# Performance work log

Hardware: AMD Instinct MI355X
Metric: run time of the kernel (lower is better)

## Reference

```python
import jax, jax.numpy as jnp
import numpy as np

EPS = 1e-5
GROUPS = 4


def gconv1x1(x, w, b, groups):
    # x: [B,C,H,W]; w: [Cout, Cin//groups]; grouped 1x1 conv
    B, C, H, W = x.shape
    Co = w.shape[0]
    xg = x.reshape(B, groups, C // groups, H, W)
    wg = w.reshape(groups, Co // groups, C // groups)
    y = jnp.einsum('bgchw,goc->bgohw', xg, wg).reshape(B, Co, H, W)
    if b is not None:
        y = y + b[None, :, None, None]
    return y


def setup_inputs() -> dict:
    key = jax.random.key(0)
    ks = jax.random.split(key, 9)
    B, C, H, W = 8, 64, 160, 160
    Cq = C // 8
    s = 0.1
    return {
        'x': jax.random.normal(ks[0], (B, C, H, W), jnp.float32),
        'wq': jax.random.normal(ks[1], (Cq, C // GROUPS), jnp.float32) * s,
        'bq': jax.random.normal(ks[2], (Cq,), jnp.float32) * s,
        'wk': jax.random.normal(ks[3], (Cq, C // GROUPS), jnp.float32) * s,
        'bk': jax.random.normal(ks[4], (Cq,), jnp.float32) * s,
        'wv': jax.random.normal(ks[5], (C, C // GROUPS), jnp.float32) * s,
        'bv': jax.random.normal(ks[6], (C,), jnp.float32) * s,
        'gamma': jax.random.normal(ks[7], (1,), jnp.float32) * s,
        'w1d': jax.random.normal(ks[8], (C, C // GROUPS), jnp.float32) * s,
        'bn_w': jnp.ones((C,), jnp.float32),
        'bn_b': jnp.zeros((C,), jnp.float32),
    }


def reference(x, wq, bq, wk, bk, wv, bv, gamma, w1d, bn_w, bn_b):
    B, C, H, W = x.shape
    q = gconv1x1(x, wq, bq, GROUPS)   # [B,Cq,H,W]
    k = gconv1x1(x, wk, bk, GROUPS)   # [B,Cq,H,W]
    v = gconv1x1(x, wv, bv, GROUPS)   # [B,C,H,W]

    # column (H) attention energies with -inf diagonal (self excluded on H path)
    energy_H = jnp.einsum('bchw,bcjw->bhwj', q, k)  # [B,H,W,H]
    diag = jnp.where(jnp.eye(H, dtype=bool), -jnp.inf, 0.0).astype(x.dtype)
    energy_H = energy_H + diag[:, None, :]
    # row (W) attention energies
    energy_W = jnp.einsum('bchw,bchj->bhwj', q, k)  # [B,H,W,W]

    att = jax.nn.softmax(jnp.concatenate([energy_H, energy_W], axis=3), axis=3)
    att_H = att[..., :H]           # [B,H,W,H]
    att_W = att[..., H:]           # [B,H,W,W]

    out_H = jnp.einsum('bcjw,bhwj->bchw', v, att_H)
    out_W = jnp.einsum('bchj,bhwj->bchw', v, att_W)
    out = gamma[0] * (out_H + out_W)               # [B,C,H,W]

    # kernel-size-1 grouped conv1d (dilation irrelevant for k=1), no bias
    L = H * W
    o = out.reshape(B, GROUPS, C // GROUPS, L)
    w1g = w1d.reshape(GROUPS, C // GROUPS, C // GROUPS)
    o = jnp.einsum('bgcl,goc->bgol', o, w1g).reshape(B, C, L)

    # BatchNorm1d (training mode: batch stats over (B, L), biased variance)
    mean = jnp.mean(o, axis=(0, 2), keepdims=True)
    var = jnp.mean((o - mean) ** 2, axis=(0, 2), keepdims=True)
    o = (o - mean) / jnp.sqrt(var + EPS) * bn_w[None, :, None] + bn_b[None, :, None]

    o = o.reshape(B, C, H, W)
    return jax.nn.relu(o + x)
```

## Files before the change

kernel.cpp:

```cpp
#include <hip/hip_runtime.h>
#include <math.h>

#define B_ 8
#define C_ 64
#define H_ 160
#define W_ 160
#define HW_ (H_*W_)

typedef _Float16 h2 __attribute__((ext_vector_type(2)));
typedef _Float16 h4 __attribute__((ext_vector_type(4)));
typedef _Float16 h8 __attribute__((ext_vector_type(8)));
typedef float f4v __attribute__((ext_vector_type(4)));
union H8u { h8 v; h2 h[4]; };

__device__ inline float fdot2(h2 a, h2 b, float c) {
    return __builtin_amdgcn_fdot2(a, b, c, false);
}

#define LOG2E 1.44269504088896f
#define ESH2  5.77078016355585f
#if __has_builtin(__builtin_amdgcn_exp2f)
#define EXP2F(x) __builtin_amdgcn_exp2f(x)
#else
#define EXP2F(x) exp2f(x)
#endif

__device__ inline void cvtw16(const float* wp, float sc, H8u& a, H8u& b) {
    #pragma unroll
    for (int j = 0; j < 4; j++) {
        float4 f = ((const float4*)wp)[j];
        h2 lo, hi;
        lo.x = (_Float16)(f.x*sc); lo.y = (_Float16)(f.y*sc);
        hi.x = (_Float16)(f.z*sc); hi.y = (_Float16)(f.w*sc);
        if (j < 2) { a.h[(j&1)*2] = lo; a.h[(j&1)*2+1] = hi; }
        else       { b.h[(j&1)*2] = lo; b.h[(j&1)*2+1] = hi; }
    }
}

static constexpr size_t N_PIX  = (size_t)B_*H_*W_;
static constexpr size_t N_FULL = (size_t)B_*H_*W_*C_;
static constexpr size_t OFF_OUTH  = 0;
static constexpr size_t OFF_VROW  = N_FULL/2;
static constexpr size_t OFF_QROW  = OFF_VROW + N_FULL/2;
static constexpr size_t OFF_KROW  = OFF_QROW + N_PIX*4;
static constexpr size_t OFF_MH    = OFF_KROW + N_PIX*4;
static constexpr size_t OFF_SH    = OFF_MH + N_PIX;
static constexpr size_t OFF_BNSUM = OFF_SH + N_PIX;
static constexpr size_t OFF_BNSQ  = OFF_BNSUM + 64;

__global__ __launch_bounds__(256,4) void qkv_kernel(
    const float* __restrict__ x,
    const float* __restrict__ wq, const float* __restrict__ bq,
    const float* __restrict__ wk, const float* __restrict__ bk,
    const float* __restrict__ wv, const float* __restrict__ bv,
    _Float16* __restrict__ qrow, _Float16* __restrict__ krow,
    _Float16* __restrict__ vrow)
{
    __shared__ __align__(16) _Float16 spool[10240];
    _Float16 (*xsh)[72] = (_Float16 (*)[72])spool;

    const int tid = threadIdx.x;
    const int w0 = blockIdx.x * 32;
    const int h0 = blockIdx.y * 4;
    const int b  = blockIdx.z;

    const float* xb = x + (size_t)b*C_*HW_;
    for (int i = tid; i < 2048; i += 256) {
        int w4 = i & 7;
        int c  = ((i >> 3) & 7) | (((i >> 6) & 7) << 3);
        int hh = i >> 9;
        float4 v = *(const float4*)(xb + (size_t)c*HW_ + (size_t)(h0+hh)*W_ + w0 + w4*4);
        int pix = hh*32 + w4*4;
        xsh[pix+0][c] = (_Float16)v.x; xsh[pix+1][c] = (_Float16)v.y;
        xsh[pix+2][c] = (_Float16)v.z; xsh[pix+3][c] = (_Float16)v.w;
    }
    __syncthreads();

    float resv[32];
    {
        const int cp = tid & 31, pg = tid >> 5;
        const int c0 = 2*cp, g = c0 >> 4;
        H8u wa0, wb0, wa1, wb1;
        cvtw16(wv + c0*16,     1.0f, wa0, wb0);
        cvtw16(wv + (c0+1)*16, 1.0f, wa1, wb1);
        const float b0 = bv[c0], b1 = bv[c0+1];
        #pragma unroll 4
        for (int i = 0; i < 16; i++) {
            int pix = pg*16 + i;
            H8u x0; x0.v = *(const h8*)&xsh[pix][g*16];
            H8u x1; x1.v = *(const h8*)&xsh[pix][g*16 + 8];
            float s0 = b0, s1 = b1;
            #pragma unroll
            for (int j = 0; j < 4; j++) {
                s0 = fdot2(x0.h[j], wa0.h[j], s0);
                s1 = fdot2(x0.h[j], wa1.h[j], s1);
            }
            #pragma unroll
            for (int j = 0; j < 4; j++) {
                s0 = fdot2(x1.h[j], wb0.h[j], s0);
                s1 = fdot2(x1.h[j], wb1.h[j], s1);
            }
            resv[2*i] = s0; resv[2*i+1] = s1;
        }
    }
    float resqk[8];
    {
        const int out = tid & 15, pg = tid >> 4;
        const int cq = out & 7, g = cq >> 1;
        const float sc = (out < 8) ? LOG2E : 1.0f;
        const float* wp = ((out < 8) ? wq : wk) + cq*16;
        const float bb = ((out < 8) ? bq[cq] : bk[cq]) * sc;
        H8u qa, qb;
        cvtw16(wp, sc, qa, qb);
        #pragma unroll
        for (int i = 0; i < 8; i++) {
            int pix = pg*8 + i;
            H8u x0; x0.v = *(const h8*)&xsh[pix][g*16];
            H8u x1; x1.v = *(const h8*)&xsh[pix][g*16 + 8];
            float s = bb;
            #pragma unroll
            for (int j = 0; j < 4; j++) s = fdot2(x0.h[j], qa.h[j], s);
            #pragma unroll
            for (int j = 0; j < 4; j++) s = fdot2(x1.h[j], qb.h[j], s);
            resqk[i] = s;
        }
    }
    __syncthreads();

    unsigned* vs32 = (unsigned*)spool;
    unsigned* qk32 = vs32 + 4096;
    {
        const int cp = tid & 31, pg = tid >> 5;
        #pragma unroll
        for (int i = 0; i < 16; i++) {
            int pix = pg*16 + i;
            h2 p; p.x = (_Float16)resv[2*i]; p.y = (_Float16)resv[2*i+1];
            vs32[pix*32 + cp] = *(unsigned*)&p;
        }
    }
    {
        const int out = tid & 15, pg = tid >> 4;
        _Float16* qks = (_Float16*)qk32;
        #pragma unroll
        for (int i = 0; i < 8; i++) qks[(pg*8+i)*16 + out] = (_Float16)resqk[i];
    }
    __syncthreads();

    unsigned* vrow32 = (unsigned*)vrow;
    for (int i = tid; i < 4096; i += 256) {
        int pix = i >> 5, cp = i & 31;
        size_t bp = ((size_t)b*H_ + h0 + (pix>>5))*W_ + w0 + (pix & 31);
        vrow32[bp*32 + cp] = vs32[i];
    }
    unsigned* qrow32 = (unsigned*)qrow;
    unsigned* krow32 = (unsigned*)krow;
    for (int i = tid; i < 1024; i += 256) {
        int pix = i >> 3, part = i & 7;
        size_t bp = ((size_t)b*H_ + h0 + (pix>>5))*W_ + w0 + (pix & 31);
        unsigned val = qk32[pix*8 + part];
        if (part < 4) qrow32[bp*4 + part]     = val;
        else          krow32[bp*4 + part - 4] = val;
    }
}

__global__ __launch_bounds__(256,4) void passA_kernel(
    const _Float16* __restrict__ qrow, const _Float16* __restrict__ krow,
    const _Float16* __restrict__ vrow,
    _Float16* __restrict__ outH, float* __restrict__ sH)
{
    __shared__ __align__(16) _Float16 pool[10240];
    __shared__ __align__(16) _Float16 q2h[160][8];
    __shared__ __align__(16) _Float16 k2h[160][8];

    _Float16* v2s = pool;

    const int tid = threadIdx.x;
    const int b = blockIdx.x / W_;
    const int w = blockIdx.x % W_;

    if (tid < 160) {
        size_t bp = ((size_t)b*H_ + tid)*W_ + w;
        *(int4*)&q2h[tid][0] = *(const int4*)(qrow + bp*8);
        *(int4*)&k2h[tid][0] = *(const int4*)(krow + bp*8);
    }
    {
        const unsigned* vr32 = (const unsigned*)vrow;
        const int cp = tid & 31, hp0 = tid >> 5;
        #pragma unroll 5
        for (int it = 0; it < 10; it++) {
            int hp = hp0 + 8*it;
            int kt = hp >> 4, dqv = (hp >> 2) & 3, jj = 2*(hp & 3);
            size_t bp0 = ((size_t)b*H_ + 2*hp)*W_ + w;
            unsigned u0 = vr32[bp0*32 + cp];
            unsigned u1 = vr32[(bp0 + W_)*32 + cp];
            unsigned e  = __builtin_amdgcn_perm(u1, u0, 0x05040100);
            unsigned o  = __builtin_amdgcn_perm(u1, u0, 0x07060302);
            int base = ((kt*4 + dqv)*64 + 2*cp)*8 + jj;
            *(unsigned*)&v2s[base]     = e;
            *(unsigned*)&v2s[base + 8] = o;
        }
    }
    __syncthreads();

    const int u    = tid & 7;
    const int wl   = tid >> 3;
    const int lane = tid & 63;
    const int wid  = tid >> 6;
    const int cM   = wid*16 + (lane & 15);
    const int m_   = lane & 15;
    const int dq   = lane >> 4;

    h8 vfr[5];
    #pragma unroll
    for (int kt = 0; kt < 5; kt++)
        vfr[kt] = *(const h8*)&v2s[((kt*4 + dq)*64 + cM)*8];
    __syncthreads();

    for (int t = 0; t <= 5; t++) {
        if (t <= 4) {
            _Float16* Pts = pool + (t & 1)*5120;
            const int qh = t*32 + wl;
            H8u qr; qr.v = *(const h8*)&q2h[qh][0];
            float sloc = 0.f;
            #pragma unroll
            for (int p = 0; p < 10; p++) {
                int j0 = 2*u + 16*p;
                H8u ka; ka.v = *(const h8*)&k2h[j0][0];
                H8u kb; kb.v = *(const h8*)&k2h[j0+1][0];
                float e0 = 0.f, e1 = 0.f;
                #pragma unroll
                for (int i = 0; i < 4; i++) {
                    e0 = fdot2(qr.h[i], ka.h[i], e0);
                    e1 = fdot2(qr.h[i], kb.h[i], e1);
                }
                float p0 = (j0   == qh) ? 0.f : EXP2F(e0 - ESH2);
                float p1 = (j0+1 == qh) ? 0.f : EXP2F(e1 - ESH2);
                sloc += p0 + p1;
                h2 pp; pp.x = (_Float16)p0; pp.y = (_Float16)p1;
                int idx = (((p>>1)*4 + (u>>2) + 2*(p&1))*32 + wl)*8 + 2*(u&3);
                *(unsigned*)&Pts[idx] = *(unsigned*)&pp;
            }
            sloc += __shfl_xor(sloc, 1);
            sloc += __shfl_xor(sloc, 2);
            sloc += __shfl_xor(sloc, 4);
            if (u == 0) sH[((size_t)b*W_ + w)*H_ + qh] = sloc;
        }
        if (t >= 1) {
            const _Float16* Pts = pool + ((t-1) & 1)*5120;
            f4v acc0 = {0.f,0.f,0.f,0.f}, acc1 = {0.f,0.f,0.f,0.f};
            #pragma unroll
            for (int kt = 0; kt < 5; kt++) {
                h8 a0  = *(const h8*)&Pts[((kt*4 + dq)*32 + m_)*8];
                h8 a1  = *(const h8*)&Pts[((kt*4 + dq)*32 + 16 + m_)*8];
                acc0 = __builtin_amdgcn_mfma_f32_16x16x32_f16(a0, vfr[kt], acc0, 0, 0, 0);
                acc1 = __builtin_amdgcn_mfma_f32_16x16x32_f16(a1, vfr[kt], acc1, 0, 0, 0);
            }
            #pragma unroll
            for (int r = 0; r < 4; r++) {
                int r0 = (t-1)*32 + dq*4 + r;
                outH[(((size_t)b*H_ + r0     )*W_ + w)*64 + cM] = (_Float16)acc0[r];
                outH[(((size_t)b*H_ + r0 + 16)*W_ + w)*64 + cM] = (_Float16)acc1[r];
            }
        }
        if (t <= 4) __syncthreads();
    }
}

__global__ __launch_bounds__(256,4) void passB_kernel(
    const _Float16* __restrict__ qrow, const _Float16* __restrict__ krow,
    const _Float16* vrow,
    const float* __restrict__ gamma, const float* __restrict__ w1d,
    const _Float16* __restrict__ outH, const float* __restrict__ sH,
    _Float16* o16, float* __restrict__ bnsum, float* __restrict__ bnsq)
{
    __shared__ __align__(16) _Float16 pool[10240];
    __shared__ __align__(16) _Float16 stageh[4*32*20];
    __shared__ __align__(16) _Float16 q2h[160][8];
    __shared__ __align__(16) _Float16 k2h[160][8];
    __shared__ float fs[2][32];

    _Float16* v2s = pool;

    const int tid = threadIdx.x;
    const int b = blockIdx.x / H_;
    const int h = blockIdx.x % H_;
    const float gam = gamma[0];

    const int lane = tid & 63;
    const int wid  = tid >> 6;
    const int cM   = wid*16 + (lane & 15);
    const int m_   = lane & 15;
    const int dq   = lane >> 4;

    h4 w1f;
    {
        float4 wv4 = *(const float4*)(w1d + cM*16 + 4*dq);
        w1f[0] = (_Float16)wv4.x; w1f[1] = (_Float16)wv4.y;
        w1f[2] = (_Float16)wv4.z; w1f[3] = (_Float16)wv4.w;
    }

    const size_t rowbase = ((size_t)b*H_ + h)*W_;
    if (tid < 160) {
        size_t bp = rowbase + tid;
        *(int4*)&q2h[tid][0] = *(const int4*)(qrow + bp*8);
        *(int4*)&k2h[tid][0] = *(const int4*)(krow + bp*8);
    }
    {
        const unsigned* vr32 = (const unsigned*)vrow;
        const int cp = tid & 31, wp0 = tid >> 5;
        #pragma unroll 5
        for (int it = 0; it < 10; it++) {
            int wp = wp0 + 8*it;
            int kt = wp >> 4, dqv = (wp >> 2) & 3, jj = 2*(wp & 3);
            size_t bp0 = rowbase + 2*wp;
            unsigned u0 = vr32[bp0*32 + cp];
            unsigned u1 = vr32[(bp0 + 1)*32 + cp];
            unsigned e  = __builtin_amdgcn_perm(u1, u0, 0x05040100);
            unsigned o  = __builtin_amdgcn_perm(u1, u0, 0x07060302);
            int base = ((kt*4 + dqv)*64 + 2*cp)*8 + jj;
            *(unsigned*)&v2s[base]     = e;
            *(unsigned*)&v2s[base + 8] = o;
        }
    }
    __syncthreads();

    const int u  = tid & 7;
    const int wl = tid >> 3;

    h8 vfr[5];
    #pragma unroll
    for (int kt = 0; kt < 5; kt++)
        vfr[kt] = *(const h8*)&v2s[((kt*4 + dq)*64 + cM)*8];
    __syncthreads();

    float bnS = 0.f, bnS2 = 0.f;

    for (int t = 0; t <= 5; t++) {
        float oh0[4], oh1[4];
        if (t >= 1) {
            #pragma unroll
            for (int r = 0; r < 4; r++) {
                int rw0 = (t-1)*32 + dq*4 + r;
                oh0[r] = (float)outH[(rowbase + rw0     )*64 + cM];
                oh1[r] = (float)outH[(rowbase + rw0 + 16)*64 + cM];
            }
        }
        if (t <= 4) {
            _Float16* Pts = pool + (t & 1)*5120;
            const int qw = t*32 + wl;
            H8u qr; qr.v = *(const h8*)&q2h[qw][0];
            float sloc = 0.f;
            #pragma unroll
            for (int p = 0; p < 10; p++) {
                int j0 = 2*u + 16*p;
                H8u ka; ka.v = *(const h8*)&k2h[j0][0];
                H8u kb; kb.v = *(const h8*)&k2h[j0+1][0];
                float e0 = 0.f, e1 = 0.f;
                #pragma unroll
                for (int i = 0; i < 4; i++) {
                    e0 = fdot2(qr.h[i], ka.h[i], e0);
                    e1 = fdot2(qr.h[i], kb.h[i], e1);
                }
                float p0 = EXP2F(e0 - ESH2);
                float p1 = EXP2F(e1 - ESH2);
                sloc += p0 + p1;
                h2 pp; pp.x = (_Float16)p0; pp.y = (_Float16)p1;
                int idx = (((p>>1)*4 + (u>>2) + 2*(p&1))*32 + wl)*8 + 2*(u&3);
                *(unsigned*)&Pts[idx] = *(unsigned*)&pp;
            }
            sloc += __shfl_xor(sloc, 1);
            sloc += __shfl_xor(sloc, 2);
            sloc += __shfl_xor(sloc, 4);
            if (u == 0) {
                float sHv = sH[((size_t)b*W_ + qw)*H_ + h];
                fs[t & 1][wl] = gam / (sHv + sloc);
            }
        }
        if (t >= 1) {
            const int tp = t - 1;
            const _Float16* Pts = pool + (tp & 1)*5120;
            const float* fr = fs[tp & 1];
            f4v acc0 = {0.f,0.f,0.f,0.f}, acc1 = {0.f,0.f,0.f,0.f};
            #pragma unroll
            for (int kt = 0; kt < 5; kt++) {
                h8 a0  = *(const h8*)&Pts[((kt*4 + dq)*32 + m_)*8];
                h8 a1  = *(const h8*)&Pts[((kt*4 + dq)*32 + 16 + m_)*8];
                acc0 = __builtin_amdgcn_mfma_f32_16x16x32_f16(a0, vfr[kt], acc0, 0, 0, 0);
                acc1 = __builtin_amdgcn_mfma_f32_16x16x32_f16(a1, vfr[kt], acc1, 0, 0, 0);
            }
            _Float16* st = &stageh[wid*640];
            #pragma unroll
            for (int r = 0; r < 4; r++) {
                int rl0 = dq*4 + r, rl1 = rl0 + 16;
                st[rl0*20 + m_] = (_Float16)((oh0[r] + acc0[r]) * fr[rl0]);
                st[rl1*20 + m_] = (_Float16)((oh1[r] + acc1[r]) * fr[rl1]);
            }
            h4 a0c = *(const h4*)&st[m_*20 + 4*dq];
            h4 a1c = *(const h4*)&st[(m_ + 16)*20 + 4*dq];
            f4v c0 = {0.f,0.f,0.f,0.f}, c1 = {0.f,0.f,0.f,0.f};
            c0 = __builtin_amdgcn_mfma_f32_16x16x16f16(a0c, w1f, c0, 0, 0, 0);
            c1 = __builtin_amdgcn_mfma_f32_16x16x16f16(a1c, w1f, c1, 0, 0, 0);
            #pragma unroll
            for (int r = 0; r < 4; r++) {
                int pr0 = dq*4 + r, pr1 = pr0 + 16;
                float o0 = c0[r], o1 = c1[r];
                o16[(rowbase + tp*32 + pr0)*64 + cM] = (_Float16)o0;
                o16[(rowbase + tp*32 + pr1)*64 + cM] = (_Float16)o1;
                bnS  += o0 + o1;
                bnS2 += o0*o0 + o1*o1;
            }
        }
        if (t <= 4) __syncthreads();
    }
    bnS  += __shfl_xor(bnS, 16);  bnS  += __shfl_xor(bnS, 32);
    bnS2 += __shfl_xor(bnS2, 16); bnS2 += __shfl_xor(bnS2, 32);
    if (dq == 0) {
        atomicAdd(&bnsum[cM], bnS);
        atomicAdd(&bnsq[cM],  bnS2);
    }
}

__global__ __launch_bounds__(256) void final_kernel(
    const float* __restrict__ x, const _Float16* __restrict__ o16,
    const float* __restrict__ bnsum, const float* __restrict__ bnsq,
    const float* __restrict__ bn_w, const float* __restrict__ bn_b,
    float* __restrict__ out)
{
    __shared__ _Float16 olds[160*66];
    __shared__ float sc[64], sh[64];
    const int tid = threadIdx.x;
    const int b = blockIdx.x / H_, h = blockIdx.x % H_;
    if (tid < 64) {
        const float cnt = (float)(B_*H_*W_);
        float mean = bnsum[tid] / cnt;
        float var  = bnsq[tid] / cnt - mean*mean;
        float istd = rsqrtf(var + 1e-5f);
        float scl  = bn_w[tid] * istd;
        sc[tid] = scl;
        sh[tid] = bn_b[tid] - mean*scl;
    }
    const unsigned* op = (const unsigned*)(o16 + ((size_t)b*H_ + h)*W_*64);
    unsigned* ol32 = (unsigned*)olds;
    for (int i = tid; i < 5120; i += 256) {
        int w = i >> 5, c2 = i & 31;
        ol32[w*33 + c2] = op[i];
    }
    __syncthreads();
    const float* xr = x   + (size_t)b*C_*HW_ + (size_t)h*W_;
    float*       ob = out + (size_t)b*C_*HW_ + (size_t)h*W_;
    for (int i = tid; i < 64*160; i += 256) {
        int c = i / 160, w = i - c*160;
        float v = (float)olds[w*66 + c] * sc[c] + sh[c] + xr[(size_t)c*HW_ + w];
        ob[(size_t)c*HW_ + w] = fmaxf(v, 0.f);
    }
}

extern "C" void kernel_launch(void* const* d_in, const int* in_sizes, int n_in,
                              void* d_out, int out_size, void* d_ws, size_t ws_size,
                              hipStream_t stream)
{
    (void)in_sizes; (void)n_in; (void)out_size; (void)ws_size;
    const float* x     = (const float*)d_in[0];
    const float* wq    = (const float*)d_in[1];
    const float* bq    = (const float*)d_in[2];
    const float* wk    = (const float*)d_in[3];
    const float* bk    = (const float*)d_in[4];
    const float* wv    = (const float*)d_in[5];
    const float* bv    = (const float*)d_in[6];
    const float* gamma = (const float*)d_in[7];
    const float* w1d   = (const float*)d_in[8];
    const float* bn_w  = (const float*)d_in[9];
    const float* bn_b  = (const float*)d_in[10];

    float* ws = (float*)d_ws;
    _Float16* outH16 = (_Float16*)(ws + OFF_OUTH);
    _Float16* vrow   = (_Float16*)(ws + OFF_VROW);
    _Float16* qrow   = (_Float16*)(ws + OFF_QROW);
    _Float16* krow   = (_Float16*)(ws + OFF_KROW);
    float* sH    = ws + OFF_SH;
    float* bnsum = ws + OFF_BNSUM;
    float* bnsq  = ws + OFF_BNSQ;
    _Float16* o16 = vrow;

    (void)hipMemsetAsync(bnsum, 0, 128*sizeof(float), stream);

    dim3 qgrid(W_/32, H_/4, B_);
    qkv_kernel<<<qgrid, 256, 0, stream>>>(x, wq, bq, wk, bk, wv, bv, qrow, krow, vrow);
    passA_kernel<<<B_*W_, 256, 0, stream>>>(qrow, krow, vrow, outH16, sH);
    passB_kernel<<<B_*H_, 256, 0, stream>>>(qrow, krow, vrow, gamma, w1d,
                                            outH16, sH, o16, bnsum, bnsq);
    final_kernel<<<B_*H_, 256, 0, stream>>>(x, o16, bnsum, bnsq, bn_w, bn_b, (float*)d_out);
}
```

Measured before the change: 221.6 us.

## Compute attention energies with MFMA instead of fdot2 in both passes

Replaces the per-thread fdot2 loop that builds Q·K energies with 16x16x16 f16 MFMA tiles. Each wave now handles 16 queries against five 16-key tiles, zero-padding the K dimension from 8 to 16. Row sums are written as partial sums to shared memory and reduced later. Pass B also preloads the sH column into shared memory once instead of reading it from global per tile, and broadcasts the normalisation factors with shuffles. The MFMA call spends half its work on zero padding, and the new P-tile write layout must match what the second MFMA stage expects.

```diff
diff --git a/kernel.cpp b/kernel.cpp
--- a/kernel.cpp
+++ b/kernel.cpp
@@ -171,6 +171,7 @@
     __shared__ __align__(16) _Float16 pool[10240];
     __shared__ __align__(16) _Float16 q2h[160][8];
     __shared__ __align__(16) _Float16 k2h[160][8];
+    __shared__ float psum2[2][2][32];
 
     _Float16* v2s = pool;
 
@@ -202,13 +203,15 @@
     }
     __syncthreads();
 
-    const int u    = tid & 7;
-    const int wl   = tid >> 3;
     const int lane = tid & 63;
     const int wid  = tid >> 6;
     const int cM   = wid*16 + (lane & 15);
     const int m_   = lane & 15;
     const int dq   = lane >> 4;
+    const int n16  = lane & 15;
+    const int kg   = lane >> 4;
+    const int qs   = wid & 1;
+    const int jt0  = (wid >> 1)*5;
 
     h8 vfr[5];
     #pragma unroll
@@ -219,33 +222,37 @@
     for (int t = 0; t <= 5; t++) {
         if (t <= 4) {
             _Float16* Pts = pool + (t & 1)*5120;
-            const int qh = t*32 + wl;
-            H8u qr; qr.v = *(const h8*)&q2h[qh][0];
-            float sloc = 0.f;
-            #pragma unroll
-            for (int p = 0; p < 10; p++) {
-                int j0 = 2*u + 16*p;
-                H8u ka; ka.v = *(const h8*)&k2h[j0][0];
-                H8u kb; kb.v = *(const h8*)&k2h[j0+1][0];
-                float e0 = 0.f, e1 = 0.f;
+            const int q32  = qs*16 + n16;
+            const int qrw  = t*32 + q32;
+            h4 qf = *(const h4*)&q2h[qrw][(kg & 1)*4];
+            if (kg >= 2) { qf[0]=(_Float16)0; qf[1]=(_Float16)0; qf[2]=(_Float16)0; qf[3]=(_Float16)0; }
+            float psloc = 0.f;
+            #pragma unroll
+            for (int jj = 0; jj < 5; jj++) {
+                const int jt = jt0 + jj;
+                h4 kf = *(const h4*)&k2h[jt*16 + n16][(kg & 1)*4];
+                f4v d = {0.f,0.f,0.f,0.f};
+                d = __builtin_amdgcn_mfma_f32_16x16x16f16(kf, qf, d, 0, 0, 0);
+                const int grp = (jt >> 1)*4 + (jt & 1)*2 + (kg >> 1);
+                h4 pk;
                 #pragma unroll
-                for (int i = 0; i < 4; i++) {
-                    e0 = fdot2(qr.h[i], ka.h[i], e0);
-                    e1 = fdot2(qr.h[i], kb.h[i], e1);
+                for (int r = 0; r < 4; r++) {
+                    float p = EXP2F(d[r] - ESH2);
+                    if (jt*16 + kg*4 + r == qrw) p = 0.f;
+                    psloc += p;
+                    pk[r] = (_Float16)p;
                 }
-                float p0 = (j0   == qh) ? 0.f : EXP2F(e0 - ESH2);
-                float p1 = (j0+1 == qh) ? 0.f : EXP2F(e1 - ESH2);
-                sloc += p0 + p1;
-                h2 pp; pp.x = (_Float16)p0; pp.y = (_Float16)p1;
-                int idx = (((p>>1)*4 + (u>>2) + 2*(p&1))*32 + wl)*8 + 2*(u&3);
-                *(unsigned*)&Pts[idx] = *(unsigned*)&pp;
-            }
-            sloc += __shfl_xor(sloc, 1);
-            sloc += __shfl_xor(sloc, 2);
-            sloc += __shfl_xor(sloc, 4);
-            if (u == 0) sH[((size_t)b*W_ + w)*H_ + qh] = sloc;
+                *(h4*)&Pts[(grp*32 + q32)*8 + (kg & 1)*4] = pk;
+            }
+            psloc += __shfl_xor(psloc, 16);
+            psloc += __shfl_xor(psloc, 32);
+            if (kg == 0) psum2[t & 1][wid >> 1][q32] = psloc;
         }
         if (t >= 1) {
+            if (tid < 32) {
+                sH[((size_t)b*W_ + w)*H_ + (t-1)*32 + tid] =
+                    psum2[(t-1) & 1][0][tid] + psum2[(t-1) & 1][1][tid];
+            }
             const _Float16* Pts = pool + ((t-1) & 1)*5120;
             f4v acc0 = {0.f,0.f,0.f,0.f}, acc1 = {0.f,0.f,0.f,0.f};
             #pragma unroll
@@ -277,7 +284,8 @@
     __shared__ __align__(16) _Float16 stageh[4*32*20];
     __shared__ __align__(16) _Float16 q2h[160][8];
     __shared__ __align__(16) _Float16 k2h[160][8];
-    __shared__ float fs[2][32];
+    __shared__ float sHrow[160];
+    __shared__ float psum2[2][2][32];
 
     _Float16* v2s = pool;
 
@@ -291,6 +299,10 @@
     const int cM   = wid*16 + (lane & 15);
     const int m_   = lane & 15;
     const int dq   = lane >> 4;
+    const int n16  = lane & 15;
+    const int kg   = lane >> 4;
+    const int qs   = wid & 1;
+    const int jt0  = (wid >> 1)*5;
 
     h4 w1f;
     {
@@ -304,6 +316,7 @@
         size_t bp = rowbase + tid;
         *(int4*)&q2h[tid][0] = *(const int4*)(qrow + bp*8);
         *(int4*)&k2h[tid][0] = *(const int4*)(krow + bp*8);
+        sHrow[tid] = sH[((size_t)b*W_ + tid)*H_ + h];
     }
     {
         const unsigned* vr32 = (const unsigned*)vrow;
@@ -324,9 +337,6 @@
     }
     __syncthreads();
 
-    const int u  = tid & 7;
-    const int wl = tid >> 3;
-
     h8 vfr[5];
     #pragma unroll
     for (int kt = 0; kt < 5; kt++)
@@ -347,39 +357,37 @@
         }
         if (t <= 4) {
             _Float16* Pts = pool + (t & 1)*5120;
-            const int qw = t*32 + wl;
-            H8u qr; qr.v = *(const h8*)&q2h[qw][0];
-            float sloc = 0.f;
-            #pragma unroll
-            for (int p = 0; p < 10; p++) {
-                int j0 = 2*u + 16*p;
-                H8u ka; ka.v = *(const h8*)&k2h[j0][0];
-                H8u kb; kb.v = *(const h8*)&k2h[j0+1][0];
-                float e0 = 0.f, e1 = 0.f;
+            const int q32 = qs*16 + n16;
+            const int qrw = t*32 + q32;
+            h4 qf = *(const h4*)&q2h[qrw][(kg & 1)*4];
+            if (kg >= 2) { qf[0]=(_Float16)0; qf[1]=(_Float16)0; qf[2]=(_Float16)0; qf[3]=(_Float16)0; }
+            float psloc = 0.f;
+            #pragma unroll
+            for (int jj = 0; jj < 5; jj++) {
+                const int jt = jt0 + jj;
+                h4 kf = *(const h4*)&k2h[jt*16 + n16][(kg & 1)*4];
+                f4v d = {0.f,0.f,0.f,0.f};
+                d = __builtin_amdgcn_mfma_f32_16x16x16f16(kf, qf, d, 0, 0, 0);
+                const int grp = (jt >> 1)*4 + (jt & 1)*2 + (kg >> 1);
+                h4 pk;
                 #pragma unroll
-                for (int i = 0; i < 4; i++) {
-                    e0 = fdot2(qr.h[i], ka.h[i], e0);
-                    e1 = fdot2(qr.h[i], kb.h[i], e1);
+                for (int r = 0; r < 4; r++) {
+                    float p = EXP2F(d[r] - ESH2);
+                    psloc += p;
+                    pk[r] = (_Float16)p;
                 }
-                float p0 = EXP2F(e0 - ESH2);
-                float p1 = EXP2F(e1 - ESH2);
-                sloc += p0 + p1;
-                h2 pp; pp.x = (_Float16)p0; pp.y = (_Float16)p1;
-                int idx = (((p>>1)*4 + (u>>2) + 2*(p&1))*32 + wl)*8 + 2*(u&3);
-                *(unsigned*)&Pts[idx] = *(unsigned*)&pp;
-            }
-            sloc += __shfl_xor(sloc, 1);
-            sloc += __shfl_xor(sloc, 2);
-            sloc += __shfl_xor(sloc, 4);
-            if (u == 0) {
-                float sHv = sH[((size_t)b*W_ + qw)*H_ + h];
-                fs[t & 1][wl] = gam / (sHv + sloc);
-            }
+                *(h4*)&Pts[(grp*32 + q32)*8 + (kg & 1)*4] = pk;
+            }
+            psloc += __shfl_xor(psloc, 16);
+            psloc += __shfl_xor(psloc, 32);
+            if (kg == 0) psum2[t & 1][wid >> 1][q32] = psloc;
         }
         if (t >= 1) {
             const int tp = t - 1;
             const _Float16* Pts = pool + (tp & 1)*5120;
-            const float* fr = fs[tp & 1];
+            const int rl_ = lane & 31;
+            float fval = gam / (sHrow[tp*32 + rl_]
+                                + psum2[tp & 1][0][rl_] + psum2[tp & 1][1][rl_]);
             f4v acc0 = {0.f,0.f,0.f,0.f}, acc1 = {0.f,0.f,0.f,0.f};
             #pragma unroll
             for (int kt = 0; kt < 5; kt++) {
@@ -392,8 +400,10 @@
             #pragma unroll
             for (int r = 0; r < 4; r++) {
                 int rl0 = dq*4 + r, rl1 = rl0 + 16;
-                st[rl0*20 + m_] = (_Float16)((oh0[r] + acc0[r]) * fr[rl0]);
-                st[rl1*20 + m_] = (_Float16)((oh1[r] + acc1[r]) * fr[rl1]);
+                float f0 = __shfl(fval, rl0);
+                float f1 = __shfl(fval, rl1);
+                st[rl0*20 + m_] = (_Float16)((oh0[r] + acc0[r]) * f0);
+                st[rl1*20 + m_] = (_Float16)((oh1[r] + acc1[r]) * f1);
             }
             h4 a0c = *(const h4*)&st[m_*20 + 4*dq];
             h4 a1c = *(const h4*)&st[(m_ + 16)*20 + 4*dq];
```

Measured after the change: 214.0 us. 3.4% less time.
